# Optimization experiments

Hardware: AMD Instinct MI355X
Metric: run time of the kernel (lower is better)

The kernel has to match this reference:

```python
import jax, jax.numpy as jnp
import numpy as np
from jax import lax

DEC = [256, 128, 64, 32]
INS = [512, 256, 128, 64]


def _conv2d(x, w, b, pad):
    y = lax.conv_general_dilated(x, w, (1, 1), [(pad, pad), (pad, pad)],
                                 dimension_numbers=('NCHW', 'OIHW', 'NCHW'))
    return y + b[None, :, None, None]


def _conv_transpose2d(x, w_t, b):
    # torch ConvTranspose2d(k=3, stride=2, padding=1, output_padding=1): H -> 2H
    # equivalent to lhs-dilated conv with spatially flipped, IO-transposed kernel
    w = jnp.flip(jnp.transpose(w_t, (1, 0, 2, 3)), (2, 3))  # [out, in, 3, 3]
    y = lax.conv_general_dilated(x, w, (1, 1), [(1, 2), (1, 2)],
                                 lhs_dilation=(2, 2),
                                 dimension_numbers=('NCHW', 'OIHW', 'NCHW'))
    return y + b[None, :, None, None]


def setup_inputs() -> dict:
    key = jax.random.key(0)
    ks = iter(jax.random.split(key, 40))
    d = {}
    d['enc_feat'] = jax.random.normal(next(ks), (8, 512, 16, 16), jnp.float32)
    d['semantic_map'] = jax.random.normal(next(ks), (8, 32, 256, 256), jnp.float32)

    def w(k, shape, fan_in):
        return jax.random.normal(k, shape, jnp.float32) / np.float32(np.sqrt(fan_in))

    for i in range(4):
        d['wt%d' % i] = w(next(ks), (INS[i], DEC[i], 3, 3), INS[i] * 9)  # torch convT layout [in,out,kh,kw]
        d['bt%d' % i] = jnp.zeros((DEC[i],), jnp.float32)
        d['wc%d' % i] = w(next(ks), (DEC[i], DEC[i], 3, 3), DEC[i] * 9)
        d['bc%d' % i] = jnp.zeros((DEC[i],), jnp.float32)
    d['w_attn'] = w(next(ks), (16, 32, 1, 1), 32)
    d['b_attn'] = jnp.zeros((16,), jnp.float32)
    d['w_fin'] = w(next(ks), (1, 16, 1, 1), 16)
    d['b_fin'] = jnp.zeros((1,), jnp.float32)
    return d


def _forward(enc_feat, semantic_map, wts, bts, wcs, bcs, w_attn, b_attn, w_fin, b_fin):
    x = enc_feat
    for i in range(4):
        x = jax.nn.elu(_conv_transpose2d(x, wts[i], bts[i]))
        x = jax.nn.elu(_conv2d(x, wcs[i], bcs[i], 1))
        # skip concats are zero-channel in the only executable config -> identity
    # DynamicSemanticAttention (channel attention over C' = in_ch // 2)
    q = _conv2d(x, w_attn, b_attn, 0)                 # [B, 16, H, W]
    kf = _conv2d(semantic_map, w_attn, b_attn, 0)     # [B, 16, H, W]
    B, C, H, W = q.shape
    qf = q.reshape(B, C, H * W)                        # [B, C', N]
    attn = jnp.einsum('bcn,bdn->bcd', qf, kf.reshape(B, C, H * W))  # [B, C', C']
    attn = jax.nn.softmax(attn, axis=-1)
    fused = jnp.einsum('bcd,bdn->bcn', attn, qf).reshape(B, C, H, W) + q
    return jax.nn.sigmoid(_conv2d(fused, w_fin, b_fin, 0))  # [B, 1, H, W]


def reference(enc_feat, semantic_map, wt0, bt0, wc0, bc0, wt1, bt1, wc1, bc1,
              wt2, bt2, wc2, bc2, wt3, bt3, wc3, bc3, w_attn, b_attn, w_fin, b_fin):
    wts = [wt0, wt1, wt2, wt3]
    bts = [bt0, bt1, bt2, bt3]
    wcs = [wc0, wc1, wc2, wc3]
    bcs = [bc0, bc1, bc2, bc3]
    return _forward(enc_feat, semantic_map, wts, bts, wcs, bcs,
                    w_attn, b_attn, w_fin, b_fin)
```

## Files before the change

kernel.cpp:

```cpp
#include <hip/hip_runtime.h>
#include <hip/hip_bf16.h>
#include <math.h>

typedef _Float16 f16;
typedef _Float16 h8 __attribute__((ext_vector_type(8)));
typedef _Float16 h4 __attribute__((ext_vector_type(4)));
typedef float    f4 __attribute__((ext_vector_type(4)));

__device__ __forceinline__ float elu_f(float v) { return v > 0.f ? v : __expf(v) - 1.f; }
__device__ __forceinline__ float sigmoid_f(float v) { return 1.f / (1.f + __expf(-v)); }

struct PrepDesc { const float* src; unsigned dstOff; int OC; int IC; int tr; };
struct P8 { PrepDesc d[8]; };

__global__ void prep_all_k(P8 p, f16* __restrict__ wp,
                           const float* __restrict__ enc, f16* __restrict__ enc_cl) {
    __shared__ float ts[32][257];
    if (blockIdx.x < 128) {
        const int b = blockIdx.x >> 4, cg = blockIdx.x & 15;
        const int tid = threadIdx.x;
        #pragma unroll
        for (int i = 0; i < 32; ++i)
            ts[i][tid] = enc[((size_t)(b * 512 + cg * 32 + i)) * 256 + tid];
        __syncthreads();
        #pragma unroll
        for (int k = 0; k < 4; ++k) {
            h8 v;
            #pragma unroll
            for (int q = 0; q < 8; ++q) v[q] = (f16)ts[k * 8 + q][tid];
            *(h8*)(enc_cl + ((size_t)(b * 256 + tid)) * 512 + cg * 32 + k * 8) = v;
        }
        return;
    }
    unsigned idx = (blockIdx.x - 128) * 256u + threadIdx.x;
    for (int s = 0; s < 8; ++s) {
        const int IC = p.d[s].IC, OC = p.d[s].OC;
        const unsigned cnt = (unsigned)(OC * 9 * IC);
        if (idx < cnt) {
            const int nicc = IC >> 5;
            const int j    = idx & 7;
            const int lane = (idx >> 3) & 63;
            const int mt   = (idx >> 9) & 1;
            unsigned r = idx >> 10;
            const int tap = r % 9;  r /= 9;
            const int icchunk = r % nicc;
            const int ocg     = r / nicc;
            const int oc = ocg * 32 + mt * 16 + (lane & 15);
            const int ic = icchunk * 32 + (lane >> 4) * 8 + j;
            const float v = p.d[s].tr ? p.d[s].src[((size_t)ic * OC + oc) * 9 + tap]
                                      : p.d[s].src[((size_t)oc * IC + ic) * 9 + tap];
            wp[p.d[s].dstOff + idx] = (f16)v;
            return;
        }
        idx -= cnt;
    }
}

template<int SKS>
__device__ __forceinline__ h8 stage_elem(const f16* __restrict__ in, size_t off,
                                         size_t srcTot, const float* __restrict__ sbias,
                                         int ch0) {
    if constexpr (SKS == 1) {
        return *(const h8*)(in + off);
    } else {
        float s[8];
        const h8 t0 = *(const h8*)(in + off);
        #pragma unroll
        for (int j = 0; j < 8; ++j) s[j] = (float)t0[j];
        #pragma unroll
        for (int k = 1; k < SKS; ++k) {
            const h8 tk = *(const h8*)(in + (size_t)k * srcTot + off);
            #pragma unroll
            for (int j = 0; j < 8; ++j) s[j] += (float)tk[j];
        }
        const float4 b0 = *(const float4*)(sbias + ch0);
        const float4 b1 = *(const float4*)(sbias + ch0 + 4);
        h8 v;
        v[0] = (f16)elu_f(s[0] + b0.x); v[1] = (f16)elu_f(s[1] + b0.y);
        v[2] = (f16)elu_f(s[2] + b0.z); v[3] = (f16)elu_f(s[3] + b0.w);
        v[4] = (f16)elu_f(s[4] + b1.x); v[5] = (f16)elu_f(s[5] + b1.y);
        v[6] = (f16)elu_f(s[6] + b1.z); v[7] = (f16)elu_f(s[7] + b1.w);
        return v;
    }
}

template<int C, int H, int W, int HT, int WT, int NWN, int KS, int SKS>
__launch_bounds__(256, 2)
__global__ void conv3_mfma(const f16* __restrict__ in, const f16* __restrict__ wp,
                           const float* __restrict__ bias, const float* __restrict__ sbias,
                           size_t srcTot, f16* __restrict__ out, f16* __restrict__ pout) {
    constexpr int NWR = 4 / NWN;
    constexpr int RH  = HT / NWR;
    constexpr int PIXR = WT + 2;
    constexpr int ROWS = HT + 2;
    constexpr int XB = ROWS * PIXR * 80;
    constexpr int NICC = C / 32;
    constexpr int XTILES = W / WT;
    constexpr int NLD = ROWS * PIXR * 4;
    constexpr int NIT = (NLD + 255) / 256;
    constexpr int CPB = C / KS / 32;
    __shared__ __align__(16) char xlds[XB];

    const int tid = threadIdx.x;
    const int wid = tid >> 6, lane = tid & 63;
    const int ln15 = lane & 15, lg = lane >> 4;
    const int ni = wid % NWN, ri = wid / NWN;
    const int bz = blockIdx.z;
    const int bb = bz / (C / 32), ocg = bz % (C / 32);
    const int oc0 = ocg * 32;
    const int bx = blockIdx.x;
    const int xt = bx % XTILES, ks = bx / XTILES;
    const int h0 = blockIdx.y * HT, w0 = xt * WT;
    const int colb = ni * 16 + ln15;

    f4 acc[RH][2] = {};

    auto compute_chunk = [&](int icc) {
        const f16* wbl = wp + ((size_t)(ocg * NICC + (icc >> 5)) * 18) * 512 + lane * 8;
        #pragma unroll
        for (int dw = 0; dw < 3; ++dw) {
            h8 afd[3][2];
            #pragma unroll
            for (int dh = 0; dh < 3; ++dh)
                #pragma unroll
                for (int mt = 0; mt < 2; ++mt)
                    afd[dh][mt] = *(const h8*)(wbl + ((dh * 3 + dw) * 2 + mt) * 512);
            h8 bfv[RH + 2];
            #pragma unroll
            for (int q = 0; q < RH + 2; ++q)
                bfv[q] = *(const h8*)(xlds + ((ri * RH + q) * PIXR + colb + dw) * 80 + lg * 16);
            #pragma unroll
            for (int r = 0; r < RH; ++r) {
                #pragma unroll
                for (int dh = 0; dh < 3; ++dh) {
                    acc[r][0] = __builtin_amdgcn_mfma_f32_16x16x32_f16(afd[dh][0], bfv[r + dh], acc[r][0], 0, 0, 0);
                    acc[r][1] = __builtin_amdgcn_mfma_f32_16x16x32_f16(afd[dh][1], bfv[r + dh], acc[r][1], 0, 0, 0);
                }
            }
        }
    };

    if constexpr (SKS == 1 && CPB > 1) {
        h8 pre[NIT];
        const int icc0 = ks * (C / KS);
        auto do_loads = [&](int icc) {
            #pragma unroll
            for (int i = 0; i < NIT; ++i) {
                const int t = tid + i * 256;
                if (t < NLD) {
                    const int g = t & 3, pix = t >> 2;
                    const int rr = pix / PIXR, ww = pix - rr * PIXR;
                    const int gh = h0 - 1 + rr, gw = w0 - 1 + ww;
                    h8 v = {};
                    if (gh >= 0 && gh < H && gw >= 0 && gw < W)
                        v = *(const h8*)(in + (((size_t)bb * H + gh) * W + gw) * C + icc + g * 8);
                    pre[i] = v;
                }
            }
        };
        do_loads(icc0);
        for (int ci = 0; ci < CPB; ++ci) {
            __syncthreads();
            #pragma unroll
            for (int i = 0; i < NIT; ++i) {
                const int t = tid + i * 256;
                if (t < NLD) {
                    const int g = t & 3, pix = t >> 2;
                    *(h8*)(xlds + pix * 80 + g * 16) = pre[i];
                }
            }
            __syncthreads();
            if (ci + 1 < CPB) do_loads(icc0 + (ci + 1) * 32);
            compute_chunk(icc0 + ci * 32);
        }
    } else {
        for (int icc = ks * (C / KS); icc < (ks + 1) * (C / KS); icc += 32) {
            __syncthreads();
            for (int t = tid; t < NLD; t += 256) {
                const int g = t & 3, pix = t >> 2;
                const int rr = pix / PIXR, ww = pix - rr * PIXR;
                const int gh = h0 - 1 + rr, gw = w0 - 1 + ww;
                h8 v = {};
                if (gh >= 0 && gh < H && gw >= 0 && gw < W) {
                    const size_t off = (((size_t)bb * H + gh) * W + gw) * C + icc + g * 8;
                    v = stage_elem<SKS>(in, off, srcTot, sbias, icc + g * 8);
                }
                *(h8*)(xlds + pix * 80 + g * 16) = v;
            }
            __syncthreads();
            compute_chunk(icc);
        }
    }

    #pragma unroll
    for (int r = 0; r < RH; ++r) {
        const int oh = h0 + ri * RH + r;
        const int ow = w0 + colb;
        #pragma unroll
        for (int mt = 0; mt < 2; ++mt) {
            const int ocl = mt * 16 + lg * 4;
            const f4 v = acc[r][mt];
            if constexpr (KS > 1) {
                const size_t TOT = (size_t)8 * H * W * C;
                h4 hv = {(f16)v.x, (f16)v.y, (f16)v.z, (f16)v.w};
                *(h4*)(pout + (size_t)ks * TOT +
                       (((size_t)bb * H + oh) * W + ow) * C + oc0 + ocl) = hv;
            } else {
                const float4 b4 = *(const float4*)(bias + oc0 + ocl);
                h4 hv = {(f16)elu_f(v.x + b4.x), (f16)elu_f(v.y + b4.y),
                         (f16)elu_f(v.z + b4.z), (f16)elu_f(v.w + b4.w)};
                *(h4*)(out + (((size_t)bb * H + oh) * W + ow) * C + oc0 + ocl) = hv;
            }
        }
    }
}

template<int IC, int OC, int Hi, int Wi, int KS, int SKS>
__launch_bounds__(256, 2)
__global__ void convt_mfma(const f16* __restrict__ in, const f16* __restrict__ wp,
                           const float* __restrict__ bias, const float* __restrict__ sbias,
                           size_t srcTot, f16* __restrict__ out, f16* __restrict__ pout) {
    constexpr int HT = 4, WT = 16;
    constexpr int PIXR = WT + 1;
    constexpr int ROWS = HT + 1;
    constexpr int XB = ROWS * PIXR * 80;
    constexpr int NICC = IC / 32;
    constexpr int XTILES = Wi / WT;
    constexpr int NLD = ROWS * PIXR * 4;
    constexpr int NIT = (NLD + 255) / 256;
    constexpr int CPB = IC / KS / 32;
    __shared__ __align__(16) char xlds[XB];

    const int tid = threadIdx.x;
    const int wid = tid >> 6, lane = tid & 63;
    const int ln15 = lane & 15, lg = lane >> 4;
    const int iloc = wid;
    const int bz = blockIdx.z;
    const int bb = bz / (OC / 32), ocg = bz % (OC / 32);
    const int oc0 = ocg * 32;
    const int bx = blockIdx.x;
    const int xt = bx % XTILES, ks = bx / XTILES;
    const int i0 = blockIdx.y * HT, j0 = xt * WT;

    f4 acc[4][2] = {};

    auto compute_chunk = [&](int icc) {
        const f16* wbl = wp + ((size_t)(ocg * NICC + (icc >> 5)) * 18) * 512 + lane * 8;
        h8 af[9][2];
        #pragma unroll
        for (int tap = 0; tap < 9; ++tap)
            #pragma unroll
            for (int mt = 0; mt < 2; ++mt)
                af[tap][mt] = *(const h8*)(wbl + (tap * 2 + mt) * 512);

        h8 bf[2][2];
        #pragma unroll
        for (int a = 0; a < 2; ++a)
            #pragma unroll
            for (int b = 0; b < 2; ++b)
                bf[a][b] = *(const h8*)(xlds + ((iloc + a) * PIXR + ln15 + b) * 80 + lg * 16);

        #pragma unroll
        for (int p = 0; p < 4; ++p) {
            const int di = p >> 1, dj = p & 1;
            #pragma unroll
            for (int a = 0; a < 2; ++a) {
                if (a > di) continue;
                const int kh = 1 + di - 2 * a;
                #pragma unroll
                for (int b = 0; b < 2; ++b) {
                    if (b > dj) continue;
                    const int kw = 1 + dj - 2 * b;
                    const int tap = kh * 3 + kw;
                    acc[p][0] = __builtin_amdgcn_mfma_f32_16x16x32_f16(af[tap][0], bf[a][b], acc[p][0], 0, 0, 0);
                    acc[p][1] = __builtin_amdgcn_mfma_f32_16x16x32_f16(af[tap][1], bf[a][b], acc[p][1], 0, 0, 0);
                }
            }
        }
    };

    if constexpr (SKS == 1 && CPB > 1) {
        h8 pre[NIT];
        const int icc0 = ks * (IC / KS);
        auto do_loads = [&](int icc) {
            #pragma unroll
            for (int i = 0; i < NIT; ++i) {
                const int t = tid + i * 256;
                if (t < NLD) {
                    const int g = t & 3, pix = t >> 2;
                    const int rr = pix / PIXR, ww = pix - rr * PIXR;
                    const int gh = i0 + rr, gw = j0 + ww;
                    h8 v = {};
                    if (gh < Hi && gw < Wi)
                        v = *(const h8*)(in + (((size_t)bb * Hi + gh) * Wi + gw) * IC + icc + g * 8);
                    pre[i] = v;
                }
            }
        };
        do_loads(icc0);
        for (int ci = 0; ci < CPB; ++ci) {
            __syncthreads();
            #pragma unroll
            for (int i = 0; i < NIT; ++i) {
                const int t = tid + i * 256;
                if (t < NLD) {
                    const int g = t & 3, pix = t >> 2;
                    *(h8*)(xlds + pix * 80 + g * 16) = pre[i];
                }
            }
            __syncthreads();
            if (ci + 1 < CPB) do_loads(icc0 + (ci + 1) * 32);
            compute_chunk(icc0 + ci * 32);
        }
    } else {
        for (int icc = ks * (IC / KS); icc < (ks + 1) * (IC / KS); icc += 32) {
            __syncthreads();
            for (int t = tid; t < NLD; t += 256) {
                const int g = t & 3, pix = t >> 2;
                const int rr = pix / PIXR, ww = pix - rr * PIXR;
                const int gh = i0 + rr, gw = j0 + ww;
                h8 v = {};
                if (gh < Hi && gw < Wi) {
                    const size_t off = (((size_t)bb * Hi + gh) * Wi + gw) * IC + icc + g * 8;
                    v = stage_elem<SKS>(in, off, srcTot, sbias, icc + g * 8);
                }
                *(h8*)(xlds + pix * 80 + g * 16) = v;
            }
            __syncthreads();
            compute_chunk(icc);
        }
    }

    #pragma unroll
    for (int p = 0; p < 4; ++p) {
        const int orow = 2 * (i0 + iloc) + (p >> 1);
        const int ocol = 2 * (j0 + ln15) + (p & 1);
        #pragma unroll
        for (int mt = 0; mt < 2; ++mt) {
            const int ocl = mt * 16 + lg * 4;
            const f4 v = acc[p][mt];
            if constexpr (KS > 1) {
                const size_t TOT = (size_t)8 * (2 * Hi) * (2 * Wi) * OC;
                h4 hv = {(f16)v.x, (f16)v.y, (f16)v.z, (f16)v.w};
                *(h4*)(pout + (size_t)ks * TOT +
                       (((size_t)bb * (2 * Hi) + orow) * (2 * Wi) + ocol) * OC + oc0 + ocl) = hv;
            } else {
                const float4 b4 = *(const float4*)(bias + oc0 + ocl);
                h4 hv = {(f16)elu_f(v.x + b4.x), (f16)elu_f(v.y + b4.y),
                         (f16)elu_f(v.z + b4.z), (f16)elu_f(v.w + b4.w)};
                *(h4*)(out + (((size_t)bb * (2 * Hi) + orow) * (2 * Wi) + ocol) * OC + oc0 + ocl) = hv;
            }
        }
    }
}

__launch_bounds__(256, 2)
__global__ void conv3_gram_k(const f16* __restrict__ in, const f16* __restrict__ wp,
                             const float* __restrict__ bias, const float* __restrict__ sem,
                             f16* __restrict__ out, float* __restrict__ part,
                             float* __restrict__ sums) {
    constexpr int C = 32, H = 256, W = 256, HT = 4, WT = 64;
    constexpr int PIXR = WT + 2;
    constexpr int ROWS = HT + 2;
    constexpr int XB = ROWS * PIXR * 80;
    constexpr int X3B = 32 * 264 * 2;
    constexpr int LDSB = X3B + 16384 + 1024;
    __shared__ __align__(16) char lds[(XB > LDSB) ? XB : LDSB];
    char* xlds = lds;
    f16*   x3l = (f16*)lds;
    float* pl  = (float*)(lds + X3B);
    float* sl  = (float*)(lds + X3B + 16384);

    const int tid = threadIdx.x;
    const int wid = tid >> 6, lane = tid & 63;
    const int ln15 = lane & 15, lg = lane >> 4;
    const int ni = wid;
    const int bb = blockIdx.z;
    const int h0 = blockIdx.y * HT, w0 = blockIdx.x * WT;
    const int colb = ni * 16 + ln15;

    for (int t = tid; t < ROWS * PIXR * 4; t += 256) {
        const int g = t & 3, pix = t >> 2;
        const int rr = pix / PIXR, ww = pix - rr * PIXR;
        const int gh = h0 - 1 + rr, gw = w0 - 1 + ww;
        h8 v = {};
        if (gh >= 0 && gh < H && gw >= 0 && gw < W)
            v = *(const h8*)(in + (((size_t)bb * H + gh) * W + gw) * C + g * 8);
        *(h8*)(xlds + pix * 80 + g * 16) = v;
    }

    const int row = ln15, kg = lg;
    const size_t N = 65536;
    const float* sb = sem + ((size_t)bb * 32 + row) * N + (size_t)(h0 + wid) * 256 + w0 + kg * 8;
    float4 semr[8];
    #pragma unroll
    for (int ks2 = 0; ks2 < 2; ++ks2) {
        const int k0 = ks2 * 32;
        semr[ks2 * 4 + 0] = *(const float4*)(sb + k0);
        semr[ks2 * 4 + 1] = *(const float4*)(sb + k0 + 4);
        semr[ks2 * 4 + 2] = *(const float4*)(sb + 16 * N + k0);
        semr[ks2 * 4 + 3] = *(const float4*)(sb + 16 * N + k0 + 4);
    }
    __syncthreads();

    f4 acc[4][2] = {};
    const f16* wbl = wp + lane * 8;
    #pragma unroll
    for (int dw = 0; dw < 3; ++dw) {
        h8 afd[3][2];
        #pragma unroll
        for (int dh = 0; dh < 3; ++dh)
            #pragma unroll
            for (int mt = 0; mt < 2; ++mt)
                afd[dh][mt] = *(const h8*)(wbl + ((dh * 3 + dw) * 2 + mt) * 512);
        h8 bfv[6];
        #pragma unroll
        for (int q = 0; q < 6; ++q)
            bfv[q] = *(const h8*)(xlds + (q * PIXR + colb + dw) * 80 + lg * 16);
        #pragma unroll
        for (int r = 0; r < 4; ++r) {
            #pragma unroll
            for (int dh = 0; dh < 3; ++dh) {
                acc[r][0] = __builtin_amdgcn_mfma_f32_16x16x32_f16(afd[dh][0], bfv[r + dh], acc[r][0], 0, 0, 0);
                acc[r][1] = __builtin_amdgcn_mfma_f32_16x16x32_f16(afd[dh][1], bfv[r + dh], acc[r][1], 0, 0, 0);
            }
        }
    }
    __syncthreads();

    #pragma unroll
    for (int r = 0; r < 4; ++r) {
        const int oh = h0 + r, ow = w0 + colb;
        const int px = r * 64 + colb;
        #pragma unroll
        for (int mt = 0; mt < 2; ++mt) {
            const int ocl = mt * 16 + lg * 4;
            const float4 b4 = *(const float4*)(bias + ocl);
            const f4 v = acc[r][mt];
            h4 hv = {(f16)elu_f(v.x + b4.x), (f16)elu_f(v.y + b4.y),
                     (f16)elu_f(v.z + b4.z), (f16)elu_f(v.w + b4.w)};
            *(h4*)(out + (((size_t)bb * H + oh) * W + ow) * C + ocl) = hv;
            x3l[(ocl + 0) * 264 + px] = hv[0];
            x3l[(ocl + 1) * 264 + px] = hv[1];
            x3l[(ocl + 2) * 264 + px] = hv[2];
            x3l[(ocl + 3) * 264 + px] = hv[3];
        }
    }
    __syncthreads();

    f4 g00 = {}, g01 = {}, g10 = {}, g11 = {};
    float sx0 = 0.f, sx1 = 0.f, ss0 = 0.f, ss1 = 0.f;

    #pragma unroll
    for (int ks2 = 0; ks2 < 2; ++ks2) {
        const int k0 = ks2 * 32;
        const h8 a0 = *(const h8*)(x3l + row * 264 + wid * 64 + k0 + kg * 8);
        const h8 a1 = *(const h8*)(x3l + (row + 16) * 264 + wid * 64 + k0 + kg * 8);
        const float4 f0 = semr[ks2 * 4 + 0];
        const float4 f1 = semr[ks2 * 4 + 1];
        const float4 q0 = semr[ks2 * 4 + 2];
        const float4 q1 = semr[ks2 * 4 + 3];
        const h8 b0 = {(f16)f0.x, (f16)f0.y, (f16)f0.z, (f16)f0.w,
                       (f16)f1.x, (f16)f1.y, (f16)f1.z, (f16)f1.w};
        const h8 b1 = {(f16)q0.x, (f16)q0.y, (f16)q0.z, (f16)q0.w,
                       (f16)q1.x, (f16)q1.y, (f16)q1.z, (f16)q1.w};
        g00 = __builtin_amdgcn_mfma_f32_16x16x32_f16(a0, b0, g00, 0, 0, 0);
        g01 = __builtin_amdgcn_mfma_f32_16x16x32_f16(a0, b1, g01, 0, 0, 0);
        g10 = __builtin_amdgcn_mfma_f32_16x16x32_f16(a1, b0, g10, 0, 0, 0);
        g11 = __builtin_amdgcn_mfma_f32_16x16x32_f16(a1, b1, g11, 0, 0, 0);
        #pragma unroll
        for (int q = 0; q < 8; ++q) { sx0 += (float)a0[q]; sx1 += (float)a1[q]; }
        ss0 += (f0.x + f0.y + f0.z + f0.w) + (f1.x + f1.y + f1.z + f1.w);
        ss1 += (q0.x + q0.y + q0.z + q0.w) + (q1.x + q1.y + q1.z + q1.w);
    }

    sx0 += __shfl_xor(sx0, 16); sx0 += __shfl_xor(sx0, 32);
    sx1 += __shfl_xor(sx1, 16); sx1 += __shfl_xor(sx1, 32);
    ss0 += __shfl_xor(ss0, 16); ss0 += __shfl_xor(ss0, 32);
    ss1 += __shfl_xor(ss1, 16); ss1 += __shfl_xor(ss1, 32);

    #pragma unroll
    for (int reg = 0; reg < 4; ++reg) {
        const int c0 = 4 * kg + reg;
        pl[wid * 1024 + c0 * 32 + row]             = g00[reg];
        pl[wid * 1024 + c0 * 32 + 16 + row]        = g01[reg];
        pl[wid * 1024 + (16 + c0) * 32 + row]      = g10[reg];
        pl[wid * 1024 + (16 + c0) * 32 + 16 + row] = g11[reg];
    }
    if (lane < 16) {
        sl[wid * 64 + row]      = sx0;
        sl[wid * 64 + 16 + row] = sx1;
        sl[wid * 64 + 32 + row] = ss0;
        sl[wid * 64 + 48 + row] = ss1;
    }
    __syncthreads();

    const int chunk = blockIdx.y * 4 + blockIdx.x;
    float* pb = part + ((size_t)bb * 256 + chunk) * 1024;
    for (int t = tid; t < 1024; t += 256)
        pb[t] = pl[t] + pl[1024 + t] + pl[2048 + t] + pl[3072 + t];
    if (tid < 64)
        sums[((size_t)bb * 256 + chunk) * 64 + tid] = sl[tid] + sl[64 + tid] + sl[128 + tid] + sl[192 + tid];
}

__launch_bounds__(256)
__global__ void gram_reduce_k(const float* __restrict__ part, const float* __restrict__ sums,
                              float* __restrict__ part2, float* __restrict__ sums2) {
    const int b = blockIdx.y, g = blockIdx.x;
    const int tid = threadIdx.x;
    const int i4 = tid * 4;
    f4 a = {};
    #pragma unroll 4
    for (int ch = 0; ch < 32; ++ch) {
        const f4 v = *(const f4*)(part + ((size_t)b * 256 + g * 32 + ch) * 1024 + i4);
        a.x += v.x; a.y += v.y; a.z += v.z; a.w += v.w;
    }
    *(f4*)(part2 + ((size_t)b * 8 + g) * 1024 + i4) = a;
    if (tid < 64) {
        float s = 0.f;
        #pragma unroll 4
        for (int ch = 0; ch < 32; ++ch) s += sums[((size_t)b * 256 + g * 32 + ch) * 64 + tid];
        sums2[((size_t)b * 8 + g) * 64 + tid] = s;
    }
}

__launch_bounds__(256)
__global__ void attn_finish_v3(const float* __restrict__ part, const float* __restrict__ sums,
                               const float* __restrict__ wa, const float* __restrict__ ba,
                               const float* __restrict__ wf, const float* __restrict__ bf,
                               float* __restrict__ u, float* __restrict__ cb) {
    __shared__ float G[32][33];
    __shared__ float T[16][33];
    __shared__ float A[16][17];
    __shared__ float Sx[32], Ss[32], px[16], ps[16], v[16];
    const int b = blockIdx.x, tid = threadIdx.x;

    float a4[4] = {0.f, 0.f, 0.f, 0.f};
    for (int p = 0; p < 8; ++p) {
        const float* pp = part + ((size_t)b * 8 + p) * 1024 + tid;
        a4[0] += pp[0]; a4[1] += pp[256]; a4[2] += pp[512]; a4[3] += pp[768];
    }
    #pragma unroll
    for (int q = 0; q < 4; ++q) {
        const int t = tid + q * 256;
        G[t >> 5][t & 31] = a4[q];
    }
    if (tid < 64) {
        float s = 0.f;
        for (int p = 0; p < 8; ++p) s += sums[((size_t)b * 8 + p) * 64 + tid];
        if (tid < 32) Sx[tid] = s; else Ss[tid - 32] = s;
    }
    __syncthreads();
    for (int t = tid; t < 512; t += 256) {
        const int c = t >> 5, f = t & 31;
        float s = 0.f;
        #pragma unroll
        for (int e = 0; e < 32; ++e) s = fmaf(wa[c * 32 + e], G[e][f], s);
        T[c][f] = s;
    }
    if (tid < 32) {
        const int c = tid & 15;
        const float* S = (tid < 16) ? Sx : Ss;
        float s = 0.f;
        #pragma unroll
        for (int e = 0; e < 32; ++e) s = fmaf(wa[c * 32 + e], S[e], s);
        if (tid < 16) px[c] = s; else ps[c] = s;
    }
    __syncthreads();
    {
        const int c = tid >> 4, d = tid & 15;
        float s = 0.f;
        #pragma unroll
        for (int f2 = 0; f2 < 32; ++f2) s = fmaf(T[c][f2], wa[d * 32 + f2], s);
        s += px[c] * ba[d] + ba[c] * ps[d] + 65536.f * ba[c] * ba[d];
        A[c][d] = s;
    }
    __syncthreads();
    if (tid < 16) {
        float m = A[tid][0];
        #pragma unroll
        for (int d = 1; d < 16; ++d) m = fmaxf(m, A[tid][d]);
        float s = 0.f;
        #pragma unroll
        for (int d = 0; d < 16; ++d) { const float e = __expf(A[tid][d] - m); A[tid][d] = e; s += e; }
        const float inv = 1.f / s;
        #pragma unroll
        for (int d = 0; d < 16; ++d) A[tid][d] *= inv;
    }
    __syncthreads();
    if (tid < 16) {
        float s = wf[tid];
        #pragma unroll
        for (int c = 0; c < 16; ++c) s = fmaf(wf[c], A[c][tid], s);
        v[tid] = s;
    }
    __syncthreads();
    if (tid < 32) {
        float s = 0.f;
        #pragma unroll
        for (int d = 0; d < 16; ++d) s = fmaf(v[d], wa[d * 32 + tid], s);
        u[b * 32 + tid] = s;
    }
    if (tid == 0) {
        float s2 = bf[0];
        #pragma unroll
        for (int d = 0; d < 16; ++d) s2 = fmaf(v[d], ba[d], s2);
        cb[b] = s2;
    }
}

__launch_bounds__(256)
__global__ void final_k(const f16* __restrict__ x3, const float* __restrict__ u,
                        const float* __restrict__ cb, float* __restrict__ out) {
    const int b = blockIdx.y;
    const int nn = blockIdx.x * 256 + threadIdx.x;
    const f16* xb = x3 + ((size_t)b * 65536 + nn) * 32;
    const float* ub = u + b * 32;
    float acc = cb[b];
    #pragma unroll
    for (int g = 0; g < 4; ++g) {
        const h8 v = *(const h8*)(xb + g * 8);
        #pragma unroll
        for (int q = 0; q < 8; ++q) acc = fmaf(ub[g * 8 + q], (float)v[q], acc);
    }
    out[(size_t)b * 65536 + nn] = sigmoid_f(acc);
}

extern "C" void kernel_launch(void* const* d_in, const int* in_sizes, int n_in,
                              void* d_out, int out_size, void* d_ws, size_t ws_size,
                              hipStream_t stream) {
    const float* enc   = (const float*)d_in[0];
    const float* sem   = (const float*)d_in[1];
    const float* wt0   = (const float*)d_in[2];
    const float* bt0   = (const float*)d_in[3];
    const float* wc0   = (const float*)d_in[4];
    const float* bc0   = (const float*)d_in[5];
    const float* wt1   = (const float*)d_in[6];
    const float* bt1   = (const float*)d_in[7];
    const float* wc1   = (const float*)d_in[8];
    const float* bc1   = (const float*)d_in[9];
    const float* wt2   = (const float*)d_in[10];
    const float* bt2   = (const float*)d_in[11];
    const float* wc2   = (const float*)d_in[12];
    const float* bc2   = (const float*)d_in[13];
    const float* wt3   = (const float*)d_in[14];
    const float* bt3   = (const float*)d_in[15];
    const float* wc3   = (const float*)d_in[16];
    const float* bc3   = (const float*)d_in[17];
    const float* wattn = (const float*)d_in[18];
    const float* battn = (const float*)d_in[19];
    const float* wfin  = (const float*)d_in[20];
    const float* bfin  = (const float*)d_in[21];

    char* W = (char*)d_ws;
    f16*   actA   = (f16*)(W + 0);
    f16*   actB   = (f16*)(W + 33554432);
    f16*   x3cl   = (f16*)(W + 67108864);
    f16*   wp     = (f16*)(W + 100663296);
    f16*   enc_cl = (f16*)(W + 105906176);
    float* part   = (float*)(W + 108003328);
    float* sums   = (float*)(W + 116391936);
    float* part2  = (float*)(W + 116916224);
    float* sums2  = (float*)(W + 117178368);
    float* u      = (float*)(W + 117194752);
    float* cb     = (float*)(W + 117195776);
    float* out    = (float*)d_out;
    f16* pfA = actA;
    f16* pfB = actB;

    P8 p;
    p.d[0] = {wt0, 0u,       256, 512, 1};
    p.d[1] = {wc0, 1179648u, 256, 256, 0};
    p.d[2] = {wt1, 1769472u, 128, 256, 1};
    p.d[3] = {wc1, 2064384u, 128, 128, 0};
    p.d[4] = {wt2, 2211840u,  64, 128, 1};
    p.d[5] = {wc2, 2285568u,  64,  64, 0};
    p.d[6] = {wt3, 2322432u,  32,  64, 1};
    p.d[7] = {wc3, 2340864u,  32,  32, 0};
    prep_all_k<<<9308, 256, 0, stream>>>(p, wp, enc, enc_cl);

    convt_mfma<512, 256, 16, 16, 4, 1><<<dim3(4, 4, 64), 256, 0, stream>>>(
        enc_cl, wp, nullptr, nullptr, 0, nullptr, pfA);
    conv3_mfma<256, 32, 32, 8, 32, 2, 4, 4><<<dim3(4, 4, 64), 256, 0, stream>>>(
        pfA, wp + 1179648, nullptr, bt0, 2097152, nullptr, pfB);
    convt_mfma<256, 128, 32, 32, 2, 4><<<dim3(4, 8, 32), 256, 0, stream>>>(
        pfB, wp + 1769472, nullptr, bc0, 2097152, nullptr, pfA);
    conv3_mfma<128, 64, 64, 4, 64, 4, 2, 2><<<dim3(2, 16, 32), 256, 0, stream>>>(
        pfA, wp + 2064384, nullptr, bt1, 4194304, nullptr, pfB);
    convt_mfma<128, 64, 64, 64, 1, 2><<<dim3(4, 16, 16), 256, 0, stream>>>(
        pfB, wp + 2211840, bt2, bc1, 4194304, actA, nullptr);
    conv3_mfma<64, 128, 128, 4, 64, 4, 1, 1><<<dim3(2, 32, 16), 256, 0, stream>>>(
        actA, wp + 2285568, bc2, nullptr, 0, actB, nullptr);
    convt_mfma<64, 32, 128, 128, 1, 1><<<dim3(8, 32, 8), 256, 0, stream>>>(
        actB, wp + 2322432, bt3, nullptr, 0, actA, nullptr);
    conv3_gram_k<<<dim3(4, 64, 8), 256, 0, stream>>>(
        actA, wp + 2340864, bc3, sem, x3cl, part, sums);

    gram_reduce_k<<<dim3(8, 8), 256, 0, stream>>>(part, sums, part2, sums2);
    attn_finish_v3<<<8, 256, 0, stream>>>(part2, sums2, wattn, battn, wfin, bfin, u, cb);
    final_k<<<dim3(256, 8), 256, 0, stream>>>(x3cl, u, cb, out);
}
```

Before: 221.3 us.

## Fold gram partial reduction into attention kernel and shrink conv3_gram LDS

The separate gram_reduce kernel is removed. attn_all_k now sums all 256 per-chunk partial Gram matrices and channel sums directly, which saves one launch and the intermediate part2/sums2 buffers. In conv3_gram_k the partial-sum scratch now reuses the start of the shared buffer instead of a separate region past the x3 staging area, with an added barrier. This cuts static LDS to the input-tile size. The cost is that the whole reduction now runs on only 8 blocks, each reading roughly 1 MB serially, so it is much less parallel than the 64-block reduction it replaces.

```diff
diff --git a/kernel.cpp b/kernel.cpp
--- a/kernel.cpp
+++ b/kernel.cpp
@@ -363,13 +363,11 @@
     constexpr int PIXR = WT + 2;
     constexpr int ROWS = HT + 2;
     constexpr int XB = ROWS * PIXR * 80;
-    constexpr int X3B = 32 * 264 * 2;
-    constexpr int LDSB = X3B + 16384 + 1024;
-    __shared__ __align__(16) char lds[(XB > LDSB) ? XB : LDSB];
+    __shared__ __align__(16) char lds[XB];
     char* xlds = lds;
     f16*   x3l = (f16*)lds;
-    float* pl  = (float*)(lds + X3B);
-    float* sl  = (float*)(lds + X3B + 16384);
+    float* pl  = (float*)lds;
+    float* sl  = (float*)(lds + 16384);
 
     const int tid = threadIdx.x;
     const int wid = tid >> 6, lane = tid & 63;
@@ -479,6 +477,8 @@
     ss0 += __shfl_xor(ss0, 16); ss0 += __shfl_xor(ss0, 32);
     ss1 += __shfl_xor(ss1, 16); ss1 += __shfl_xor(ss1, 32);
 
+    __syncthreads();
+
     #pragma unroll
     for (int reg = 0; reg < 4; ++reg) {
         const int c0 = 4 * kg + reg;
@@ -504,31 +504,10 @@
 }
 
 __launch_bounds__(256)
-__global__ void gram_reduce_k(const float* __restrict__ part, const float* __restrict__ sums,
-                              float* __restrict__ part2, float* __restrict__ sums2) {
-    const int b = blockIdx.y, g = blockIdx.x;
-    const int tid = threadIdx.x;
-    const int i4 = tid * 4;
-    f4 a = {};
-    #pragma unroll 4
-    for (int ch = 0; ch < 32; ++ch) {
-        const f4 v = *(const f4*)(part + ((size_t)b * 256 + g * 32 + ch) * 1024 + i4);
-        a.x += v.x; a.y += v.y; a.z += v.z; a.w += v.w;
-    }
-    *(f4*)(part2 + ((size_t)b * 8 + g) * 1024 + i4) = a;
-    if (tid < 64) {
-        float s = 0.f;
-        #pragma unroll 4
-        for (int ch = 0; ch < 32; ++ch) s += sums[((size_t)b * 256 + g * 32 + ch) * 64 + tid];
-        sums2[((size_t)b * 8 + g) * 64 + tid] = s;
-    }
-}
-
-__launch_bounds__(256)
-__global__ void attn_finish_v3(const float* __restrict__ part, const float* __restrict__ sums,
-                               const float* __restrict__ wa, const float* __restrict__ ba,
-                               const float* __restrict__ wf, const float* __restrict__ bf,
-                               float* __restrict__ u, float* __restrict__ cb) {
+__global__ void attn_all_k(const float* __restrict__ part, const float* __restrict__ sums,
+                           const float* __restrict__ wa, const float* __restrict__ ba,
+                           const float* __restrict__ wf, const float* __restrict__ bf,
+                           float* __restrict__ u, float* __restrict__ cb) {
     __shared__ float G[32][33];
     __shared__ float T[16][33];
     __shared__ float A[16][17];
@@ -536,8 +515,9 @@
     const int b = blockIdx.x, tid = threadIdx.x;
 
     float a4[4] = {0.f, 0.f, 0.f, 0.f};
-    for (int p = 0; p < 8; ++p) {
-        const float* pp = part + ((size_t)b * 8 + p) * 1024 + tid;
+    #pragma unroll 4
+    for (int ch = 0; ch < 256; ++ch) {
+        const float* pp = part + ((size_t)b * 256 + ch) * 1024 + tid;
         a4[0] += pp[0]; a4[1] += pp[256]; a4[2] += pp[512]; a4[3] += pp[768];
     }
     #pragma unroll
@@ -547,7 +527,8 @@
     }
     if (tid < 64) {
         float s = 0.f;
-        for (int p = 0; p < 8; ++p) s += sums[((size_t)b * 8 + p) * 64 + tid];
+        #pragma unroll 4
+        for (int ch = 0; ch < 256; ++ch) s += sums[((size_t)b * 256 + ch) * 64 + tid];
         if (tid < 32) Sx[tid] = s; else Ss[tid - 32] = s;
     }
     __syncthreads();
@@ -660,8 +641,6 @@
     f16*   enc_cl = (f16*)(W + 105906176);
     float* part   = (float*)(W + 108003328);
     float* sums   = (float*)(W + 116391936);
-    float* part2  = (float*)(W + 116916224);
-    float* sums2  = (float*)(W + 117178368);
     float* u      = (float*)(W + 117194752);
     float* cb     = (float*)(W + 117195776);
     float* out    = (float*)d_out;
@@ -696,7 +675,6 @@
     conv3_gram_k<<<dim3(4, 64, 8), 256, 0, stream>>>(
         actA, wp + 2340864, bc3, sem, x3cl, part, sums);
 
-    gram_reduce_k<<<dim3(8, 8), 256, 0, stream>>>(part, sums, part2, sums2);
-    attn_finish_v3<<<8, 256, 0, stream>>>(part2, sums2, wattn, battn, wfin, bfin, u, cb);
+    attn_all_k<<<8, 256, 0, stream>>>(part, sums, wattn, battn, wfin, bfin, u, cb);
     final_k<<<dim3(256, 8), 256, 0, stream>>>(x3cl, u, cb, out);
 }
```

New measurement: 253.7 us. 1.15x slower.
